# Kernel optimization log

Hardware: AMD Instinct MI355X
Metric: run time of the kernel (lower is better)

The kernel has to match this reference:

```python
import jax, jax.numpy as jnp
import numpy as np

N_NODES = 50000
N_EDGES = 800000
HIDDEN = 128
IN_DIM = 128
OUT_DIM = 40
N_LAYERS = 3


def setup_inputs() -> dict:
    key = jax.random.key(0)
    ks = jax.random.split(key, 8)
    s = 1.0 / np.sqrt(HIDDEN)
    return {
        "x": jax.random.normal(ks[0], (N_NODES, IN_DIM), jnp.float32),
        "edge_index": jax.random.randint(ks[1], (2, N_EDGES), 0, N_NODES, jnp.int32),
        "W_in": jax.random.normal(ks[2], (IN_DIM, HIDDEN), jnp.float32) * s,
        "b_in": jnp.zeros((HIDDEN,), jnp.float32),
        "Wl": jax.random.normal(ks[3], (N_LAYERS, HIDDEN, HIDDEN), jnp.float32) * s,
        "Wr": jax.random.normal(ks[4], (N_LAYERS, HIDDEN, HIDDEN), jnp.float32) * s,
        "bl": jnp.zeros((N_LAYERS, HIDDEN), jnp.float32),
        "Wc1": jax.random.normal(ks[5], (HIDDEN, HIDDEN), jnp.float32) * s,
        "bc1": jnp.zeros((HIDDEN,), jnp.float32),
        "Wc2": jax.random.normal(ks[6], (HIDDEN, OUT_DIM), jnp.float32) * s,
        "bc2": jnp.zeros((OUT_DIM,), jnp.float32),
    }


def reference(x, edge_index, W_in, b_in, Wl, Wr, bl, Wc1, bc1, Wc2, bc2):
    src, dst = edge_index[0], edge_index[1]
    n = x.shape[0]
    # in-degree for mean aggregation (clamped to 1 for isolated nodes)
    deg = jax.ops.segment_sum(jnp.ones_like(src, x.dtype), dst, num_segments=n)
    deg_inv = (1.0 / jnp.maximum(deg, 1.0))[:, None]  # [N,1]

    h = x @ W_in + b_in  # lin1; dropout is identity in eval mode
    js = []
    for i in range(N_LAYERS):
        # GraphSAGE-mean: gather neighbor feats, scatter-mean, self + neighbor linear
        agg = jax.ops.segment_sum(h[src], dst, num_segments=n) * deg_inv
        h = jax.nn.relu(h @ Wl[i] + agg @ Wr[i] + bl[i])
        js.append(h)  # skip ops are identity; fix_last appends last layer directly

    x5 = js[0] + js[1] + js[2]  # layer aggregator 'l_sum' with linear activation
    hc = jax.nn.relu(x5 @ Wc1 + bc1)
    return hc @ Wc2 + bc2  # logits [N, OUT_DIM]
```

## Files before the change

kernel.cpp:

```cpp
#include <hip/hip_runtime.h>

#define NN   50000
#define NE   800000
#define HID  128
#define OUTD 40
#define NBLK 196

typedef float f32x4  __attribute__((ext_vector_type(4)));
typedef int   i32x4  __attribute__((ext_vector_type(4)));
typedef short bf16x8 __attribute__((ext_vector_type(8)));

__device__ __forceinline__ f32x4 mfma(bf16x8 a, bf16x8 b, f32x4 c) {
  return __builtin_amdgcn_mfma_f32_16x16x32_bf16(a, b, c, 0, 0, 0);
}
__device__ __forceinline__ unsigned short f2bf(float f) {
  unsigned u = __builtin_bit_cast(unsigned, f);
  u += 0x7fffu + ((u >> 16) & 1u);
  return (unsigned short)(u >> 16);
}
__device__ __forceinline__ unsigned pack2(float lo, float hi) {
  return (unsigned)f2bf(lo) | ((unsigned)f2bf(hi) << 16);
}
__device__ __forceinline__ float bflo(unsigned v){ return __builtin_bit_cast(float, v << 16); }
__device__ __forceinline__ float bfhi(unsigned v){ return __builtin_bit_cast(float, v & 0xffff0000u); }

__global__ void k_deg(const int* __restrict__ dst, int* __restrict__ deg,
                      int* __restrict__ pos) {
  int i = blockIdx.x * blockDim.x + threadIdx.x;
  if (i < NE) pos[i] = atomicAdd(&deg[dst[i]], 1);
}

__global__ void k_blocksum(const int* __restrict__ deg, int* __restrict__ bsum) {
  __shared__ int s[256];
  int t = threadIdx.x, i = blockIdx.x * 256 + t;
  s[t] = (i < NN) ? deg[i] : 0;
  __syncthreads();
  for (int o = 128; o > 0; o >>= 1) { if (t < o) s[t] += s[t + o]; __syncthreads(); }
  if (t == 0) bsum[blockIdx.x] = s[0];
}

__global__ void k_scan3(const int* __restrict__ deg, const int* __restrict__ bsum,
                        int* __restrict__ offs, float* __restrict__ dinv) {
  __shared__ int sb[256];
  __shared__ int s[256];
  int t = threadIdx.x, i = blockIdx.x * 256 + t;
  sb[t] = (t < NBLK && t < blockIdx.x) ? bsum[t] : 0;
  int v = (i < NN) ? deg[i] : 0;
  s[t] = v;
  __syncthreads();
  for (int o = 128; o > 0; o >>= 1) { if (t < o) sb[t] += sb[t + o]; __syncthreads(); }
  for (int o = 1; o < 256; o <<= 1) {
    int x = (t >= o) ? s[t - o] : 0;
    __syncthreads(); s[t] += x; __syncthreads();
  }
  int off = sb[0] + s[t] - v;
  if (i < NN) {
    offs[i] = off;
    dinv[i] = 1.0f / (float)(v > 0 ? v : 1);
  }
  if (i == 0) offs[NN] = NE;
}

__global__ void k_fill(const int* __restrict__ src, const int* __restrict__ dst,
                       const int* __restrict__ pos, const int* __restrict__ offs,
                       int* __restrict__ csr) {
  int i = blockIdx.x * blockDim.x + threadIdx.x;
  if (i < NE) {
    csr[offs[dst[i]] + pos[i]] = src[i];
  }
}

__global__ void k_prep(const float* __restrict__ Win, const float* __restrict__ Wl,
                       const float* __restrict__ Wr, const float* __restrict__ Wc1,
                       const float* __restrict__ Wc2, unsigned short* __restrict__ wt,
                       int* __restrict__ deg) {
  int idx = blockIdx.x * 256 + threadIdx.x;
  if (idx < NN) deg[idx] = 0;
  const int NMAIN = 8 * 16384;
  if (idx >= NMAIN + 48 * 128) return;
  float v;
  if (idx < NMAIN) {
    int m = idx >> 14, rem = idx & 16383;
    int n = rem >> 7, k = rem & 127;
    const float* s;
    if (m == 0) s = Win;
    else if (m <= 3) s = Wl + (m - 1) * 16384;
    else if (m <= 6) s = Wr + (m - 4) * 16384;
    else s = Wc1;
    v = s[k * 128 + n];
  } else {
    int rem = idx - NMAIN;
    int n = rem >> 7, k = rem & 127;
    v = (n < OUTD) ? Wc2[k * OUTD + n] : 0.f;
  }
  wt[idx] = f2bf(v);
}

__global__ __launch_bounds__(256) void k_agg(const unsigned short* __restrict__ h,
                                             const int* __restrict__ csr,
                                             const int* __restrict__ offs,
                                             const float* __restrict__ dinv,
                                             unsigned short* __restrict__ agg) {
  const int lane = threadIdx.x & 63;
  const int l31 = lane & 31;
  const int hi = lane >> 5;
  int gw = (blockIdx.x * blockDim.x + threadIdx.x) >> 6;
  int nw = (gridDim.x * blockDim.x) >> 6;
  const uint2* h2 = (const uint2*)h;
  uint2* ag2 = (uint2*)agg;
  for (int n = gw; n < NN; n += nw) {
    int s = offs[n], e = offs[n + 1];
    float a0 = 0, a1 = 0, a2 = 0, a3 = 0;
    float b0 = 0, b1 = 0, b2 = 0, b3 = 0;
    float c0 = 0, c1 = 0, c2 = 0, c3 = 0;
    float d0 = 0, d1 = 0, d2 = 0, d3 = 0;
    int k = s;
    int r0, r1, r2, r3;
    bool have = (k + 8 <= e);
    if (have) {
      r0 = csr[k + 0 + hi]; r1 = csr[k + 2 + hi];
      r2 = csr[k + 4 + hi]; r3 = csr[k + 6 + hi];
    }
    while (have) {
      uint2 v0 = h2[r0 * 32 + l31];
      uint2 v1 = h2[r1 * 32 + l31];
      uint2 v2 = h2[r2 * 32 + l31];
      uint2 v3 = h2[r3 * 32 + l31];
      k += 8;
      have = (k + 8 <= e);
      if (have) {
        r0 = csr[k + 0 + hi]; r1 = csr[k + 2 + hi];
        r2 = csr[k + 4 + hi]; r3 = csr[k + 6 + hi];
      }
      a0 += bflo(v0.x); a1 += bfhi(v0.x); a2 += bflo(v0.y); a3 += bfhi(v0.y);
      b0 += bflo(v1.x); b1 += bfhi(v1.x); b2 += bflo(v1.y); b3 += bfhi(v1.y);
      c0 += bflo(v2.x); c1 += bfhi(v2.x); c2 += bflo(v2.y); c3 += bfhi(v2.y);
      d0 += bflo(v3.x); d1 += bfhi(v3.x); d2 += bflo(v3.y); d3 += bfhi(v3.y);
    }
    for (; k + 2 <= e; k += 2) {
      int r = csr[k + hi];
      uint2 v = h2[r * 32 + l31];
      a0 += bflo(v.x); a1 += bfhi(v.x); a2 += bflo(v.y); a3 += bfhi(v.y);
    }
    if (k < e) {
      int r = csr[k];
      uint2 v = h2[r * 32 + l31];
      if (hi == 0) {
        a0 += bflo(v.x); a1 += bfhi(v.x); a2 += bflo(v.y); a3 += bfhi(v.y);
      }
    }
    float s0 = a0 + b0 + c0 + d0, s1 = a1 + b1 + c1 + d1;
    float s2 = a2 + b2 + c2 + d2, s3 = a3 + b3 + c3 + d3;
    s0 += __shfl_xor(s0, 32); s1 += __shfl_xor(s1, 32);
    s2 += __shfl_xor(s2, 32); s3 += __shfl_xor(s3, 32);
    float di = dinv[n];
    if (hi == 0) {
      uint2 o;
      o.x = pack2(s0 * di, s1 * di);
      o.y = pack2(s2 * di, s3 * di);
      ag2[n * 32 + l31] = o;
    }
  }
}

__global__ __launch_bounds__(256) void k_lin_in(const float* __restrict__ x,
                                                const unsigned short* __restrict__ Wt,
                                                const float* __restrict__ bias,
                                                unsigned short* __restrict__ hout) {
  const int lane = threadIdx.x & 63, w = threadIdx.x >> 6;
  const int wr = w >> 1, wc = w & 1;
  const int r15 = lane & 15, khi = lane >> 4;
  const int mbase = blockIdx.x * 128 + wr * 64, nbase = wc * 64;
  f32x4 acc[4][4] = {};
#pragma unroll
  for (int ks = 0; ks < 4; ++ks) {
    const int kk = ks * 32 + khi * 8;
    bf16x8 af[4], bq[4];
#pragma unroll
    for (int i = 0; i < 4; i++) {
      int row = mbase + i * 16 + r15; row = row < NN ? row : NN - 1;
      const f32x4* p = (const f32x4*)(x + row * HID + kk);
      f32x4 lo = p[0], hi = p[1];
      i32x4 t;
      t[0] = pack2(lo[0], lo[1]); t[1] = pack2(lo[2], lo[3]);
      t[2] = pack2(hi[0], hi[1]); t[3] = pack2(hi[2], hi[3]);
      af[i] = __builtin_bit_cast(bf16x8, t);
    }
#pragma unroll
    for (int j = 0; j < 4; j++) {
      int col = nbase + j * 16 + r15;
      bq[j] = *(const bf16x8*)(Wt + col * HID + kk);
    }
#pragma unroll
    for (int i = 0; i < 4; i++)
#pragma unroll
      for (int j = 0; j < 4; j++) acc[i][j] = mfma(af[i], bq[j], acc[i][j]);
  }
  float b4[4];
#pragma unroll
  for (int j = 0; j < 4; j++) b4[j] = bias[nbase + j * 16 + r15];
#pragma unroll
  for (int i = 0; i < 4; i++) {
    const int rb = mbase + i * 16 + khi * 4;
#pragma unroll
    for (int e = 0; e < 4; e++) {
      const int r = rb + e;
      if (r < NN) {
#pragma unroll
        for (int j = 0; j < 4; j++)
          hout[r * HID + nbase + j * 16 + r15] = f2bf(acc[i][j][e] + b4[j]);
      }
    }
  }
}

__global__ __launch_bounds__(256) void k_layer(const unsigned short* __restrict__ hp,
                                               const unsigned short* __restrict__ ag,
                                               const unsigned short* __restrict__ WtL,
                                               const unsigned short* __restrict__ WtR,
                                               const float* __restrict__ bias,
                                               unsigned short* __restrict__ hout) {
  const int lane = threadIdx.x & 63, w = threadIdx.x >> 6;
  const int wr = w >> 1, wc = w & 1;
  const int r15 = lane & 15, khi = lane >> 4;
  const int mbase = blockIdx.x * 128 + wr * 64, nbase = wc * 64;
  f32x4 acc[4][4] = {};
#pragma unroll
  for (int ph = 0; ph < 2; ++ph) {
    const unsigned short* A = ph ? ag : hp;
    const unsigned short* B = ph ? WtR : WtL;
#pragma unroll
    for (int ks = 0; ks < 4; ++ks) {
      const int kk = ks * 32 + khi * 8;
      bf16x8 af[4], bq[4];
#pragma unroll
      for (int i = 0; i < 4; i++) {
        int row = mbase + i * 16 + r15; row = row < NN ? row : NN - 1;
        af[i] = *(const bf16x8*)(A + row * HID + kk);
      }
#pragma unroll
      for (int j = 0; j < 4; j++) {
        int col = nbase + j * 16 + r15;
        bq[j] = *(const bf16x8*)(B + col * HID + kk);
      }
#pragma unroll
      for (int i = 0; i < 4; i++)
#pragma unroll
        for (int j = 0; j < 4; j++) acc[i][j] = mfma(af[i], bq[j], acc[i][j]);
    }
  }
  float b4[4];
#pragma unroll
  for (int j = 0; j < 4; j++) b4[j] = bias[nbase + j * 16 + r15];
#pragma unroll
  for (int i = 0; i < 4; i++) {
    const int rb = mbase + i * 16 + khi * 4;
#pragma unroll
    for (int e = 0; e < 4; e++) {
      const int r = rb + e;
      if (r < NN) {
#pragma unroll
        for (int j = 0; j < 4; j++) {
          float v = acc[i][j][e] + b4[j];
          v = fmaxf(v, 0.f);
          hout[r * HID + nbase + j * 16 + r15] = f2bf(v);
        }
      }
    }
  }
}

__global__ __launch_bounds__(256) void k_cls(const unsigned short* __restrict__ h1,
                                             const unsigned short* __restrict__ h2,
                                             const unsigned short* __restrict__ h3,
                                             const unsigned short* __restrict__ WtC1,
                                             const float* __restrict__ bc1,
                                             const unsigned short* __restrict__ WtC2,
                                             const float* __restrict__ bc2,
                                             float* __restrict__ out) {
  __shared__ unsigned short hc[128 * 136];
  const int lane = threadIdx.x & 63, w = threadIdx.x >> 6;
  const int wr = w >> 1, wc = w & 1;
  const int r15 = lane & 15, khi = lane >> 4;
  const int mbase = blockIdx.x * 128 + wr * 64, nbase = wc * 64;
  {
    f32x4 acc[4][4] = {};
#pragma unroll
    for (int ks = 0; ks < 4; ++ks) {
      const int kk = ks * 32 + khi * 8;
      bf16x8 af[4], bq[4];
#pragma unroll
      for (int i = 0; i < 4; i++) {
        int row = mbase + i * 16 + r15; row = row < NN ? row : NN - 1;
        i32x4 u = *(const i32x4*)(h1 + row * HID + kk);
        i32x4 v = *(const i32x4*)(h2 + row * HID + kk);
        i32x4 q = *(const i32x4*)(h3 + row * HID + kk);
        i32x4 t;
#pragma unroll
        for (int c = 0; c < 4; c++) {
          unsigned uu = u[c], vv = v[c], qq = q[c];
          t[c] = pack2(bflo(uu) + bflo(vv) + bflo(qq), bfhi(uu) + bfhi(vv) + bfhi(qq));
        }
        af[i] = __builtin_bit_cast(bf16x8, t);
      }
#pragma unroll
      for (int j = 0; j < 4; j++) {
        int col = nbase + j * 16 + r15;
        bq[j] = *(const bf16x8*)(WtC1 + col * HID + kk);
      }
#pragma unroll
      for (int i = 0; i < 4; i++)
#pragma unroll
        for (int j = 0; j < 4; j++) acc[i][j] = mfma(af[i], bq[j], acc[i][j]);
    }
    float b4[4];
#pragma unroll
    for (int j = 0; j < 4; j++) b4[j] = bc1[nbase + j * 16 + r15];
#pragma unroll
    for (int i = 0; i < 4; i++) {
      const int rT = wr * 64 + i * 16 + khi * 4;
#pragma unroll
      for (int e = 0; e < 4; e++) {
#pragma unroll
        for (int j = 0; j < 4; j++) {
          float v = fmaxf(acc[i][j][e] + b4[j], 0.f);
          hc[(rT + e) * 136 + nbase + j * 16 + r15] = f2bf(v);
        }
      }
    }
  }
  __syncthreads();
  {
    f32x4 a2[2][3] = {};
#pragma unroll
    for (int ks = 0; ks < 4; ++ks) {
      const int kk = ks * 32 + khi * 8;
      bf16x8 af[2], bq[3];
#pragma unroll
      for (int i = 0; i < 2; i++) {
        int rT = w * 32 + i * 16 + r15;
        af[i] = *(const bf16x8*)&hc[rT * 136 + kk];
      }
#pragma unroll
      for (int j = 0; j < 3; j++) {
        int col = j * 16 + r15;
        bq[j] = *(const bf16x8*)(WtC2 + col * HID + kk);
      }
#pragma unroll
      for (int i = 0; i < 2; i++)
#pragma unroll
        for (int j = 0; j < 3; j++) a2[i][j] = mfma(af[i], bq[j], a2[i][j]);
    }
#pragma unroll
    for (int j = 0; j < 3; j++) {
      const int col = j * 16 + r15;
      const float b = (col < OUTD) ? bc2[col] : 0.f;
#pragma unroll
      for (int i = 0; i < 2; i++) {
        const int rT = w * 32 + i * 16 + khi * 4;
#pragma unroll
        for (int e = 0; e < 4; e++) {
          const int gr = blockIdx.x * 128 + rT + e;
          if (gr < NN && col < OUTD) out[gr * OUTD + col] = a2[i][j][e] + b;
        }
      }
    }
  }
}

extern "C" void kernel_launch(void* const* d_in, const int* in_sizes, int n_in,
                              void* d_out, int out_size, void* d_ws, size_t ws_size,
                              hipStream_t stream) {
  (void)in_sizes; (void)n_in; (void)out_size; (void)ws_size;
  const float* x   = (const float*)d_in[0];
  const int*   ei  = (const int*)d_in[1];
  const float* Win = (const float*)d_in[2];
  const float* bin = (const float*)d_in[3];
  const float* Wl  = (const float*)d_in[4];
  const float* Wr  = (const float*)d_in[5];
  const float* bl  = (const float*)d_in[6];
  const float* Wc1 = (const float*)d_in[7];
  const float* bc1 = (const float*)d_in[8];
  const float* Wc2 = (const float*)d_in[9];
  const float* bc2 = (const float*)d_in[10];
  float* out = (float*)d_out;

  char* ws = (char*)d_ws;
  size_t off = 0;
  auto take = [&](size_t bytes) -> char* {
    char* p = ws + off; off = (off + bytes + 255) & ~(size_t)255; return p;
  };
  int* deg        = (int*)take((size_t)NN * 4);
  int* offs       = (int*)take((size_t)(NN + 1) * 4);
  int* pos        = (int*)take((size_t)NE * 4);
  int* bsum       = (int*)take(256 * 4);
  float* dinv     = (float*)take((size_t)NN * 4);
  int* csr        = (int*)take((size_t)NE * 4);
  unsigned short* wt  = (unsigned short*)take((size_t)(8 * 16384 + 48 * 128) * 2);
  unsigned short* h0  = (unsigned short*)take((size_t)NN * HID * 2);
  unsigned short* h1  = (unsigned short*)take((size_t)NN * HID * 2);
  unsigned short* h2  = (unsigned short*)take((size_t)NN * HID * 2);
  unsigned short* h3  = (unsigned short*)take((size_t)NN * HID * 2);
  unsigned short* agg = (unsigned short*)take((size_t)NN * HID * 2);

  const int* esrc = ei;
  const int* edst = ei + NE;

  k_prep<<<(8 * 16384 + 48 * 128 + 255) / 256, 256, 0, stream>>>(Win, Wl, Wr, Wc1, Wc2, wt, deg);
  k_deg<<<(NE + 255) / 256, 256, 0, stream>>>(edst, deg, pos);
  k_blocksum<<<NBLK, 256, 0, stream>>>(deg, bsum);
  k_scan3<<<NBLK, 256, 0, stream>>>(deg, bsum, offs, dinv);
  k_fill<<<(NE + 255) / 256, 256, 0, stream>>>(esrc, edst, pos, offs, csr);
  k_lin_in<<<(NN + 127) / 128, 256, 0, stream>>>(x, wt, bin, h0);

  unsigned short* hs[4] = {h0, h1, h2, h3};
  for (int i = 0; i < 3; i++) {
    k_agg<<<2048, 256, 0, stream>>>(hs[i], csr, offs, dinv, agg);
    k_layer<<<(NN + 127) / 128, 256, 0, stream>>>(hs[i], agg, wt + (1 + i) * 16384,
                                                  wt + (4 + i) * 16384, bl + i * HID, hs[i + 1]);
  }
  k_cls<<<(NN + 127) / 128, 256, 0, stream>>>(h1, h2, h3, wt + 7 * 16384, bc1,
                                              wt + 8 * 16384, bc2, out);
}
```

Baseline: 255.0 us.

## Merge degree count with input linear, single-block scan, deeper agg prefetch

Folds the degree-count atomics and the input linear layer into one launch by splitting blocks between the two jobs. Replaces the two-kernel block-sum/scan with a single 1024-thread block scan that also computes inverse degrees. Rewrites the aggregation loop to double-buffer neighbour feature loads two 8-edge batches ahead, and adds an occupancy hint to its launch bounds. This cuts launch count and hides gather latency, but the single-block scan serialises a pass over all nodes on one CU.

Measured after the change: 416.1 us. 1.63x slower.

```diff
diff --git a/kernel.cpp b/kernel.cpp
--- a/kernel.cpp
+++ b/kernel.cpp
@@ -4,7 +4,8 @@
 #define NE   800000
 #define HID  128
 #define OUTD 40
-#define NBLK 196
+#define DEG_BLKS ((NE + 255) / 256)
+#define LIN_BLKS ((NN + 127) / 128)
 
 typedef float f32x4  __attribute__((ext_vector_type(4)));
 typedef int   i32x4  __attribute__((ext_vector_type(4)));
@@ -23,51 +24,8 @@
 }
 __device__ __forceinline__ float bflo(unsigned v){ return __builtin_bit_cast(float, v << 16); }
 __device__ __forceinline__ float bfhi(unsigned v){ return __builtin_bit_cast(float, v & 0xffff0000u); }
-
-__global__ void k_deg(const int* __restrict__ dst, int* __restrict__ deg,
-                      int* __restrict__ pos) {
-  int i = blockIdx.x * blockDim.x + threadIdx.x;
-  if (i < NE) pos[i] = atomicAdd(&deg[dst[i]], 1);
-}
-
-__global__ void k_blocksum(const int* __restrict__ deg, int* __restrict__ bsum) {
-  __shared__ int s[256];
-  int t = threadIdx.x, i = blockIdx.x * 256 + t;
-  s[t] = (i < NN) ? deg[i] : 0;
-  __syncthreads();
-  for (int o = 128; o > 0; o >>= 1) { if (t < o) s[t] += s[t + o]; __syncthreads(); }
-  if (t == 0) bsum[blockIdx.x] = s[0];
-}
-
-__global__ void k_scan3(const int* __restrict__ deg, const int* __restrict__ bsum,
-                        int* __restrict__ offs, float* __restrict__ dinv) {
-  __shared__ int sb[256];
-  __shared__ int s[256];
-  int t = threadIdx.x, i = blockIdx.x * 256 + t;
-  sb[t] = (t < NBLK && t < blockIdx.x) ? bsum[t] : 0;
-  int v = (i < NN) ? deg[i] : 0;
-  s[t] = v;
-  __syncthreads();
-  for (int o = 128; o > 0; o >>= 1) { if (t < o) sb[t] += sb[t + o]; __syncthreads(); }
-  for (int o = 1; o < 256; o <<= 1) {
-    int x = (t >= o) ? s[t - o] : 0;
-    __syncthreads(); s[t] += x; __syncthreads();
-  }
-  int off = sb[0] + s[t] - v;
-  if (i < NN) {
-    offs[i] = off;
-    dinv[i] = 1.0f / (float)(v > 0 ? v : 1);
-  }
-  if (i == 0) offs[NN] = NE;
-}
-
-__global__ void k_fill(const int* __restrict__ src, const int* __restrict__ dst,
-                       const int* __restrict__ pos, const int* __restrict__ offs,
-                       int* __restrict__ csr) {
-  int i = blockIdx.x * blockDim.x + threadIdx.x;
-  if (i < NE) {
-    csr[offs[dst[i]] + pos[i]] = src[i];
-  }
+__device__ __forceinline__ void acc_u2(uint2 v, float& x0, float& x1, float& x2, float& x3) {
+  x0 += bflo(v.x); x1 += bfhi(v.x); x2 += bflo(v.y); x3 += bfhi(v.y);
 }
 
 __global__ void k_prep(const float* __restrict__ Win, const float* __restrict__ Wl,
@@ -96,11 +54,116 @@
   wt[idx] = f2bf(v);
 }
 
-__global__ __launch_bounds__(256) void k_agg(const unsigned short* __restrict__ h,
-                                             const int* __restrict__ csr,
-                                             const int* __restrict__ offs,
-                                             const float* __restrict__ dinv,
-                                             unsigned short* __restrict__ agg) {
+__device__ __forceinline__ void lin_in_body(int bid, const float* __restrict__ x,
+                                            const unsigned short* __restrict__ Wt,
+                                            const float* __restrict__ bias,
+                                            unsigned short* __restrict__ hout) {
+  const int lane = threadIdx.x & 63, w = threadIdx.x >> 6;
+  const int wr = w >> 1, wc = w & 1;
+  const int r15 = lane & 15, khi = lane >> 4;
+  const int mbase = bid * 128 + wr * 64, nbase = wc * 64;
+  f32x4 acc[4][4] = {};
+#pragma unroll
+  for (int ks = 0; ks < 4; ++ks) {
+    const int kk = ks * 32 + khi * 8;
+    bf16x8 af[4], bq[4];
+#pragma unroll
+    for (int i = 0; i < 4; i++) {
+      int row = mbase + i * 16 + r15; row = row < NN ? row : NN - 1;
+      const f32x4* p = (const f32x4*)(x + row * HID + kk);
+      f32x4 lo = p[0], hi = p[1];
+      i32x4 t;
+      t[0] = pack2(lo[0], lo[1]); t[1] = pack2(lo[2], lo[3]);
+      t[2] = pack2(hi[0], hi[1]); t[3] = pack2(hi[2], hi[3]);
+      af[i] = __builtin_bit_cast(bf16x8, t);
+    }
+#pragma unroll
+    for (int j = 0; j < 4; j++) {
+      int col = nbase + j * 16 + r15;
+      bq[j] = *(const bf16x8*)(Wt + col * HID + kk);
+    }
+#pragma unroll
+    for (int i = 0; i < 4; i++)
+#pragma unroll
+      for (int j = 0; j < 4; j++) acc[i][j] = mfma(af[i], bq[j], acc[i][j]);
+  }
+  float b4[4];
+#pragma unroll
+  for (int j = 0; j < 4; j++) b4[j] = bias[nbase + j * 16 + r15];
+#pragma unroll
+  for (int i = 0; i < 4; i++) {
+    const int rb = mbase + i * 16 + khi * 4;
+#pragma unroll
+    for (int e = 0; e < 4; e++) {
+      const int r = rb + e;
+      if (r < NN) {
+#pragma unroll
+        for (int j = 0; j < 4; j++)
+          hout[r * HID + nbase + j * 16 + r15] = f2bf(acc[i][j][e] + b4[j]);
+      }
+    }
+  }
+}
+
+__global__ __launch_bounds__(256) void k_deg_lin(const int* __restrict__ dst,
+                                                 int* __restrict__ deg, int* __restrict__ pos,
+                                                 const float* __restrict__ x,
+                                                 const unsigned short* __restrict__ Wt,
+                                                 const float* __restrict__ bias,
+                                                 unsigned short* __restrict__ hout) {
+  if (blockIdx.x < DEG_BLKS) {
+    int i = blockIdx.x * 256 + threadIdx.x;
+    if (i < NE) pos[i] = atomicAdd(&deg[dst[i]], 1);
+  } else {
+    lin_in_body(blockIdx.x - DEG_BLKS, x, Wt, bias, hout);
+  }
+}
+
+__global__ __launch_bounds__(1024) void k_scan_all(const int* __restrict__ deg,
+                                                   int* __restrict__ offs,
+                                                   float* __restrict__ dinv) {
+  __shared__ int part[1024];
+  const int t = threadIdx.x;
+  const int CH = (NN + 1023) / 1024;
+  const int base = t * CH;
+  int sum = 0;
+  for (int i = 0; i < CH; ++i) {
+    int idx = base + i;
+    if (idx < NN) sum += deg[idx];
+  }
+  part[t] = sum;
+  __syncthreads();
+  for (int o = 1; o < 1024; o <<= 1) {
+    int xv = (t >= o) ? part[t - o] : 0;
+    __syncthreads(); part[t] += xv; __syncthreads();
+  }
+  int running = part[t] - sum;
+  for (int i = 0; i < CH; ++i) {
+    int idx = base + i;
+    if (idx < NN) {
+      int d = deg[idx];
+      offs[idx] = running;
+      dinv[idx] = 1.0f / (float)(d > 0 ? d : 1);
+      running += d;
+    }
+  }
+  if (t == 0) offs[NN] = NE;
+}
+
+__global__ void k_fill(const int* __restrict__ src, const int* __restrict__ dst,
+                       const int* __restrict__ pos, const int* __restrict__ offs,
+                       int* __restrict__ csr) {
+  int i = blockIdx.x * blockDim.x + threadIdx.x;
+  if (i < NE) {
+    csr[offs[dst[i]] + pos[i]] = src[i];
+  }
+}
+
+__global__ __launch_bounds__(256, 6) void k_agg(const unsigned short* __restrict__ h,
+                                                const int* __restrict__ csr,
+                                                const int* __restrict__ offs,
+                                                const float* __restrict__ dinv,
+                                                unsigned short* __restrict__ agg) {
   const int lane = threadIdx.x & 63;
   const int l31 = lane & 31;
   const int hi = lane >> 5;
@@ -109,48 +172,67 @@
   const uint2* h2 = (const uint2*)h;
   uint2* ag2 = (uint2*)agg;
   for (int n = gw; n < NN; n += nw) {
-    int s = offs[n], e = offs[n + 1];
-    float a0 = 0, a1 = 0, a2 = 0, a3 = 0;
-    float b0 = 0, b1 = 0, b2 = 0, b3 = 0;
-    float c0 = 0, c1 = 0, c2 = 0, c3 = 0;
-    float d0 = 0, d1 = 0, d2 = 0, d3 = 0;
-    int k = s;
-    int r0, r1, r2, r3;
-    bool have = (k + 8 <= e);
-    if (have) {
-      r0 = csr[k + 0 + hi]; r1 = csr[k + 2 + hi];
-      r2 = csr[k + 4 + hi]; r3 = csr[k + 6 + hi];
-    }
-    while (have) {
-      uint2 v0 = h2[r0 * 32 + l31];
-      uint2 v1 = h2[r1 * 32 + l31];
-      uint2 v2 = h2[r2 * 32 + l31];
-      uint2 v3 = h2[r3 * 32 + l31];
-      k += 8;
-      have = (k + 8 <= e);
-      if (have) {
-        r0 = csr[k + 0 + hi]; r1 = csr[k + 2 + hi];
-        r2 = csr[k + 4 + hi]; r3 = csr[k + 6 + hi];
-      }
-      a0 += bflo(v0.x); a1 += bfhi(v0.x); a2 += bflo(v0.y); a3 += bfhi(v0.y);
-      b0 += bflo(v1.x); b1 += bfhi(v1.x); b2 += bflo(v1.y); b3 += bfhi(v1.y);
-      c0 += bflo(v2.x); c1 += bfhi(v2.x); c2 += bflo(v2.y); c3 += bfhi(v2.y);
-      d0 += bflo(v3.x); d1 += bfhi(v3.x); d2 += bflo(v3.y); d3 += bfhi(v3.y);
-    }
+    const int s = offs[n], e = offs[n + 1];
+    const int nb = (e - s) >> 3;
+    float p0=0,p1=0,p2=0,p3=0, q0=0,q1=0,q2=0,q3=0;
+    float u0=0,u1=0,u2=0,u3=0, w0=0,w1=0,w2=0,w3=0;
+    int ia0=0,ia1=0,ia2=0,ia3=0, ib0=0,ib1=0,ib2=0,ib3=0;
+    uint2 va0,va1,va2,va3, vb0,vb1,vb2,vb3;
+    if (nb > 0) {
+      ia0=csr[s+0+hi]; ia1=csr[s+2+hi]; ia2=csr[s+4+hi]; ia3=csr[s+6+hi];
+      va0=h2[ia0*32+l31]; va1=h2[ia1*32+l31]; va2=h2[ia2*32+l31]; va3=h2[ia3*32+l31];
+    }
+    if (nb > 1) {
+      int b1 = s + 8;
+      ib0=csr[b1+0+hi]; ib1=csr[b1+2+hi]; ib2=csr[b1+4+hi]; ib3=csr[b1+6+hi];
+      vb0=h2[ib0*32+l31]; vb1=h2[ib1*32+l31]; vb2=h2[ib2*32+l31]; vb3=h2[ib3*32+l31];
+    }
+    if (nb > 2) {
+      int b2 = s + 16;
+      ia0=csr[b2+0+hi]; ia1=csr[b2+2+hi]; ia2=csr[b2+4+hi]; ia3=csr[b2+6+hi];
+    }
+    if (nb > 3) {
+      int b3 = s + 24;
+      ib0=csr[b3+0+hi]; ib1=csr[b3+2+hi]; ib2=csr[b3+4+hi]; ib3=csr[b3+6+hi];
+    }
+    int b = 0;
+    for (; b + 2 <= nb; b += 2) {
+      acc_u2(va0, p0,p1,p2,p3); acc_u2(va1, q0,q1,q2,q3);
+      acc_u2(va2, u0,u1,u2,u3); acc_u2(va3, w0,w1,w2,w3);
+      if (b + 2 < nb) {
+        va0=h2[ia0*32+l31]; va1=h2[ia1*32+l31]; va2=h2[ia2*32+l31]; va3=h2[ia3*32+l31];
+      }
+      if (b + 4 < nb) {
+        int kk = s + ((b + 4) << 3);
+        ia0=csr[kk+0+hi]; ia1=csr[kk+2+hi]; ia2=csr[kk+4+hi]; ia3=csr[kk+6+hi];
+      }
+      acc_u2(vb0, p0,p1,p2,p3); acc_u2(vb1, q0,q1,q2,q3);
+      acc_u2(vb2, u0,u1,u2,u3); acc_u2(vb3, w0,w1,w2,w3);
+      if (b + 3 < nb) {
+        vb0=h2[ib0*32+l31]; vb1=h2[ib1*32+l31]; vb2=h2[ib2*32+l31]; vb3=h2[ib3*32+l31];
+      }
+      if (b + 5 < nb) {
+        int kk = s + ((b + 5) << 3);
+        ib0=csr[kk+0+hi]; ib1=csr[kk+2+hi]; ib2=csr[kk+4+hi]; ib3=csr[kk+6+hi];
+      }
+    }
+    if (b < nb) {
+      acc_u2(va0, p0,p1,p2,p3); acc_u2(va1, q0,q1,q2,q3);
+      acc_u2(va2, u0,u1,u2,u3); acc_u2(va3, w0,w1,w2,w3);
+    }
+    int k = s + (nb << 3);
     for (; k + 2 <= e; k += 2) {
       int r = csr[k + hi];
       uint2 v = h2[r * 32 + l31];
-      a0 += bflo(v.x); a1 += bfhi(v.x); a2 += bflo(v.y); a3 += bfhi(v.y);
+      acc_u2(v, p0,p1,p2,p3);
     }
     if (k < e) {
       int r = csr[k];
       uint2 v = h2[r * 32 + l31];
-      if (hi == 0) {
-        a0 += bflo(v.x); a1 += bfhi(v.x); a2 += bflo(v.y); a3 += bfhi(v.y);
-      }
-    }
-    float s0 = a0 + b0 + c0 + d0, s1 = a1 + b1 + c1 + d1;
-    float s2 = a2 + b2 + c2 + d2, s3 = a3 + b3 + c3 + d3;
+      if (hi == 0) acc_u2(v, p0,p1,p2,p3);
+    }
+    float s0 = (p0 + q0) + (u0 + w0), s1 = (p1 + q1) + (u1 + w1);
+    float s2 = (p2 + q2) + (u2 + w2), s3 = (p3 + q3) + (u3 + w3);
     s0 += __shfl_xor(s0, 32); s1 += __shfl_xor(s1, 32);
     s2 += __shfl_xor(s2, 32); s3 += __shfl_xor(s3, 32);
     float di = dinv[n];
@@ -159,57 +241,6 @@
       o.x = pack2(s0 * di, s1 * di);
       o.y = pack2(s2 * di, s3 * di);
       ag2[n * 32 + l31] = o;
-    }
-  }
-}
-
-__global__ __launch_bounds__(256) void k_lin_in(const float* __restrict__ x,
-                                                const unsigned short* __restrict__ Wt,
-                                                const float* __restrict__ bias,
-                                                unsigned short* __restrict__ hout) {
-  const int lane = threadIdx.x & 63, w = threadIdx.x >> 6;
-  const int wr = w >> 1, wc = w & 1;
-  const int r15 = lane & 15, khi = lane >> 4;
-  const int mbase = blockIdx.x * 128 + wr * 64, nbase = wc * 64;
-  f32x4 acc[4][4] = {};
-#pragma unroll
-  for (int ks = 0; ks < 4; ++ks) {
-    const int kk = ks * 32 + khi * 8;
-    bf16x8 af[4], bq[4];
-#pragma unroll
-    for (int i = 0; i < 4; i++) {
-      int row = mbase + i * 16 + r15; row = row < NN ? row : NN - 1;
-      const f32x4* p = (const f32x4*)(x + row * HID + kk);
-      f32x4 lo = p[0], hi = p[1];
-      i32x4 t;
-      t[0] = pack2(lo[0], lo[1]); t[1] = pack2(lo[2], lo[3]);
-      t[2] = pack2(hi[0], hi[1]); t[3] = pack2(hi[2], hi[3]);
-      af[i] = __builtin_bit_cast(bf16x8, t);
-    }
-#pragma unroll
-    for (int j = 0; j < 4; j++) {
-      int col = nbase + j * 16 + r15;
-      bq[j] = *(const bf16x8*)(Wt + col * HID + kk);
-    }
-#pragma unroll
-    for (int i = 0; i < 4; i++)
-#pragma unroll
-      for (int j = 0; j < 4; j++) acc[i][j] = mfma(af[i], bq[j], acc[i][j]);
-  }
-  float b4[4];
-#pragma unroll
-  for (int j = 0; j < 4; j++) b4[j] = bias[nbase + j * 16 + r15];
-#pragma unroll
-  for (int i = 0; i < 4; i++) {
-    const int rb = mbase + i * 16 + khi * 4;
-#pragma unroll
-    for (int e = 0; e < 4; e++) {
-      const int r = rb + e;
-      if (r < NN) {
-#pragma unroll
-        for (int j = 0; j < 4; j++)
-          hout[r * HID + nbase + j * 16 + r15] = f2bf(acc[i][j][e] + b4[j]);
-      }
     }
   }
 }
@@ -393,7 +424,6 @@
   int* deg        = (int*)take((size_t)NN * 4);
   int* offs       = (int*)take((size_t)(NN + 1) * 4);
   int* pos        = (int*)take((size_t)NE * 4);
-  int* bsum       = (int*)take(256 * 4);
   float* dinv     = (float*)take((size_t)NN * 4);
   int* csr        = (int*)take((size_t)NE * 4);
   unsigned short* wt  = (unsigned short*)take((size_t)(8 * 16384 + 48 * 128) * 2);
@@ -407,18 +437,16 @@
   const int* edst = ei + NE;
 
   k_prep<<<(8 * 16384 + 48 * 128 + 255) / 256, 256, 0, stream>>>(Win, Wl, Wr, Wc1, Wc2, wt, deg);
-  k_deg<<<(NE + 255) / 256, 256, 0, stream>>>(edst, deg, pos);
-  k_blocksum<<<NBLK, 256, 0, stream>>>(deg, bsum);
-  k_scan3<<<NBLK, 256, 0, stream>>>(deg, bsum, offs, dinv);
+  k_deg_lin<<<DEG_BLKS + LIN_BLKS, 256, 0, stream>>>(edst, deg, pos, x, wt, bin, h0);
+  k_scan_all<<<1, 1024, 0, stream>>>(deg, offs, dinv);
   k_fill<<<(NE + 255) / 256, 256, 0, stream>>>(esrc, edst, pos, offs, csr);
-  k_lin_in<<<(NN + 127) / 128, 256, 0, stream>>>(x, wt, bin, h0);
 
   unsigned short* hs[4] = {h0, h1, h2, h3};
   for (int i = 0; i < 3; i++) {
     k_agg<<<2048, 256, 0, stream>>>(hs[i], csr, offs, dinv, agg);
-    k_layer<<<(NN + 127) / 128, 256, 0, stream>>>(hs[i], agg, wt + (1 + i) * 16384,
-                                                  wt + (4 + i) * 16384, bl + i * HID, hs[i + 1]);
-  }
-  k_cls<<<(NN + 127) / 128, 256, 0, stream>>>(h1, h2, h3, wt + 7 * 16384, bc1,
-                                              wt + 8 * 16384, bc2, out);
-}
+    k_layer<<<LIN_BLKS, 256, 0, stream>>>(hs[i], agg, wt + (1 + i) * 16384,
+                                          wt + (4 + i) * 16384, bl + i * HID, hs[i + 1]);
+  }
+  k_cls<<<LIN_BLKS, 256, 0, stream>>>(h1, h2, h3, wt + 7 * 16384, bc1,
+                                      wt + 8 * 16384, bc2, out);
+}
```
